# Kernel tuning notes

Measured on AMD Instinct MI355X. Metric: run time of the kernel, lower is better.

Reference implementation:

```python
import jax, jax.numpy as jnp
import numpy as np


def position_embedding(seq_len, d):
    # inv_freq_j = 1 / 10000^(2*j/d), pos_ij = sin(i * inv_freq_j)  -> [S, d]
    inv_freq = 1.0 / jnp.power(10000.0, 2.0 * jnp.arange(d, dtype=jnp.float32) / d)
    pos = jnp.arange(seq_len, dtype=jnp.float32)
    return jnp.sin(pos[:, None] * inv_freq[None, :])  # [S, d]


def setup_inputs() -> dict:
    key = jax.random.key(0)
    k1, k2 = jax.random.split(key)
    B, S, D, OUT = 4, 4096, 64, 64
    x = jax.random.normal(k1, (B, S, D), dtype=jnp.float32)
    kernel = jax.random.normal(k2, (3, D, OUT), dtype=jnp.float32) * 0.05
    return {"x": x, "kernel": kernel}


def reference(x, kernel):
    B, S, D = x.shape
    out_dim = kernel.shape[2]
    x = x + position_embedding(S, D)[None, :, :]  # broadcast pos-embed over batch
    # stacked QKV projection: [B,S,D] x [D,out] per slot
    wq = jnp.einsum('bsd,do->bso', x, kernel[0])
    wk = jnp.einsum('bsd,do->bso', x, kernel[1])
    wv = jnp.einsum('bsd,do->bso', x, kernel[2])
    scores = jnp.einsum('bso,bto->bst', wq, wk) / jnp.sqrt(jnp.asarray(out_dim, x.dtype))
    attn = jax.nn.softmax(scores, axis=-1)  # [B,S,S]
    return jnp.einsum('bst,bto->bso', attn, wv)
```

## Files before the change

kernel.cpp:

```cpp
#include <hip/hip_runtime.h>
#include <hip/hip_bf16.h>
#include <math.h>

using bf16x8 = __attribute__((ext_vector_type(8))) __bf16;
using bf16x4 = __attribute__((ext_vector_type(4))) __bf16;
using f32x4  = __attribute__((ext_vector_type(4))) float;
using f32x16 = __attribute__((ext_vector_type(16))) float;

static constexpr int SEQ = 4096;
static constexpr int DIM = 64;
static constexpr int NB  = 4;
static constexpr float QSCALE = 0.18033688011112042f;

__device__ __forceinline__ float fast_exp2(float x) {
#if __has_builtin(__builtin_amdgcn_exp2f)
    return __builtin_amdgcn_exp2f(x);
#else
    return exp2f(x);
#endif
}

__global__ __launch_bounds__(256)
void const_prep_kernel(const float* __restrict__ w, __bf16* __restrict__ WT,
                       float* __restrict__ peb)
{
    const int idx = (int)blockIdx.x * 256 + (int)threadIdx.x;
    const int spos = idx >> 6;
    const int c    = idx & 63;
    const float invf = exp2f(-13.287712379549449f * ((float)c * 0.03125f));
    peb[idx] = __sinf((float)spos * invf);
    if (idx < 3 * DIM * DIM) {
        const int s = idx >> 12;
        const int o = (idx >> 6) & 63;
        const int d = idx & 63;
        WT[idx] = (__bf16)w[(s * DIM + d) * DIM + o];
    }
}

__global__ __launch_bounds__(256)
void qkv_prep_kernel(const float* __restrict__ x, const __bf16* __restrict__ WT,
                     const float* __restrict__ peb,
                     __bf16* __restrict__ Qf, __bf16* __restrict__ Kf,
                     __bf16* __restrict__ Vf)
{
    const int tid  = (int)threadIdx.x;
    const int lane = tid & 63;
    const int g  = lane >> 4;
    const int cl = lane & 15;
    const int rowbase = (int)blockIdx.x * 64 + (tid >> 6) * 16;

    const int row  = rowbase + cl;
    const int spos = row & (SEQ - 1);
    bf16x8 xa[2];
#pragma unroll
    for (int h = 0; h < 2; ++h) {
        const float* xp = x + (long)row * DIM + 32*h + 8*g;
        const float* pp = peb + (long)spos * DIM + 32*h + 8*g;
        f32x4 x0 = *reinterpret_cast<const f32x4*>(xp);
        f32x4 x1 = *reinterpret_cast<const f32x4*>(xp + 4);
        f32x4 p0 = *reinterpret_cast<const f32x4*>(pp);
        f32x4 p1 = *reinterpret_cast<const f32x4*>(pp + 4);
        bf16x8 v;
#pragma unroll
        for (int e = 0; e < 8; ++e) {
            const float xv = (e < 4) ? x0[e] : x1[e - 4];
            const float pe = (e < 4) ? p0[e] : p1[e - 4];
            v[e] = (__bf16)(xv + pe);
        }
        xa[h] = v;
    }

    const int bi  = rowbase >> 12;
    const int sp  = rowbase & (SEQ - 1);
    const int c32 = sp >> 5;
    const int rb16 = sp & 16;

#pragma unroll
    for (int slot = 0; slot < 3; ++slot) {
        const __bf16* wt = WT + slot * DIM * DIM;
        f32x4 acc[4];
#pragma unroll
        for (int nt = 0; nt < 4; ++nt) acc[nt] = (f32x4){0.f, 0.f, 0.f, 0.f};
#pragma unroll
        for (int nt = 0; nt < 4; ++nt) {
            bf16x8 w0 = *reinterpret_cast<const bf16x8*>(wt + (nt*16 + cl) * DIM + 8*g);
            bf16x8 w1 = *reinterpret_cast<const bf16x8*>(wt + (nt*16 + cl) * DIM + 32 + 8*g);
            if (slot < 2) {
                acc[nt] = __builtin_amdgcn_mfma_f32_16x16x32_bf16(w0, xa[0], acc[nt], 0, 0, 0);
                acc[nt] = __builtin_amdgcn_mfma_f32_16x16x32_bf16(w1, xa[1], acc[nt], 0, 0, 0);
            } else {
                acc[nt] = __builtin_amdgcn_mfma_f32_16x16x32_bf16(xa[0], w0, acc[nt], 0, 0, 0);
                acc[nt] = __builtin_amdgcn_mfma_f32_16x16x32_bf16(xa[1], w1, acc[nt], 0, 0, 0);
            }
        }

        if (slot < 2) {
            __bf16* dst = (slot == 0) ? Qf : Kf;
            const float scale = (slot == 0) ? QSCALE : 1.0f;
            __bf16* base = dst + ((long)(bi*128 + c32) * 4) * 512
                         + (rb16 + cl + 32*(g >> 1)) * 8 + 4*(g & 1);
#pragma unroll
            for (int nt = 0; nt < 4; ++nt) {
                bf16x4 pk;
#pragma unroll
                for (int r = 0; r < 4; ++r) pk[r] = (__bf16)(acc[nt][r] * scale);
                *reinterpret_cast<bf16x4*>(base + nt*512) = pk;
            }
        } else {
            const int ks  = (sp >> 4) & 1;
            const int lde = (32*(g&1) + cl)*8 + (g>>1)*4;
            __bf16* vb = Vf + (((long)bi*128 + c32)*4 + ks*2)*512;
#pragma unroll
            for (int nt = 0; nt < 4; ++nt) {
                bf16x4 pk;
#pragma unroll
                for (int r = 0; r < 4; ++r) pk[r] = (__bf16)acc[nt][r];
                *reinterpret_cast<bf16x4*>(vb + (nt>>1)*512 + (nt&1)*128 + lde) = pk;
            }
        }
    }
}

__global__ __launch_bounds__(1024)
void attn_kernel(const __bf16* __restrict__ Qf, const __bf16* __restrict__ Kf,
                 const __bf16* __restrict__ Vf, float* __restrict__ out)
{
    __shared__ char smem[71680];
    float* lpart = (float*)smem;
    float* lms   = (float*)(smem + 69632);
    float* lls   = (float*)(smem + 70656);

    const int tid  = (int)threadIdx.x;
    const int w    = tid >> 6;
    const int lane = tid & 63;
    const int hi   = lane >> 5;
    const int l31  = lane & 31;
    const int qh   = w & 1;
    const int kq   = w >> 1;

    const int bid = (int)blockIdx.x;
    const int x8  = bid & 7;
    const int b   = x8 & 3;
    const int qt64 = ((x8 >> 2) << 5) | (bid >> 3);
    const int qt32 = qt64 * 2 + qh;

    const __bf16* Qfp = Qf + ((long)(b*128 + qt32)  * 4) * 512 + lane*8;
    const __bf16* Kfp = Kf + ((long)(b*128 + kq*16) * 4) * 512 + lane*8;
    const __bf16* Vfp = Vf + ((long)(b*128 + kq*16) * 4) * 512 + lane*8;

    bf16x8 qf[4];
#pragma unroll
    for (int d4 = 0; d4 < 4; ++d4)
        qf[d4] = *reinterpret_cast<const bf16x8*>(Qfp + d4*512);

    f32x16 acc[2];
#pragma unroll
    for (int dt = 0; dt < 2; ++dt)
#pragma unroll
        for (int r = 0; r < 16; ++r) acc[dt][r] = 0.f;
    float mrun = -INFINITY;
    float lsum = 0.f;

    bf16x8 kc0 = *reinterpret_cast<const bf16x8*>(Kfp);
    bf16x8 kc1 = *reinterpret_cast<const bf16x8*>(Kfp + 512);
    bf16x8 kc2 = *reinterpret_cast<const bf16x8*>(Kfp + 1024);
    bf16x8 kc3 = *reinterpret_cast<const bf16x8*>(Kfp + 1536);

#pragma unroll 2
    for (int n = 0; n < 16; ++n) {
        bf16x8 vc0 = *reinterpret_cast<const bf16x8*>(Vfp + n*2048);
        bf16x8 vc1 = *reinterpret_cast<const bf16x8*>(Vfp + n*2048 + 512);
        bf16x8 vc2 = *reinterpret_cast<const bf16x8*>(Vfp + n*2048 + 1024);
        bf16x8 vc3 = *reinterpret_cast<const bf16x8*>(Vfp + n*2048 + 1536);
        bf16x8 kn0, kn1, kn2, kn3;
        if (n < 15) {
            kn0 = *reinterpret_cast<const bf16x8*>(Kfp + (n+1)*2048);
            kn1 = *reinterpret_cast<const bf16x8*>(Kfp + (n+1)*2048 + 512);
        }

        f32x16 s;
#pragma unroll
        for (int r = 0; r < 16; ++r) s[r] = 0.f;
        __builtin_amdgcn_s_setprio(1);
        s = __builtin_amdgcn_mfma_f32_32x32x16_bf16(kc0, qf[0], s, 0, 0, 0);
        s = __builtin_amdgcn_mfma_f32_32x32x16_bf16(kc1, qf[1], s, 0, 0, 0);
        s = __builtin_amdgcn_mfma_f32_32x32x16_bf16(kc2, qf[2], s, 0, 0, 0);
        s = __builtin_amdgcn_mfma_f32_32x32x16_bf16(kc3, qf[3], s, 0, 0, 0);
        __builtin_amdgcn_s_setprio(0);

        if (n < 15) {
            kn2 = *reinterpret_cast<const bf16x8*>(Kfp + (n+1)*2048 + 1024);
            kn3 = *reinterpret_cast<const bf16x8*>(Kfp + (n+1)*2048 + 1536);
        }

        float t0 = fmaxf(fmaxf(s[0],  s[1]),  s[2]);
        float t1 = fmaxf(fmaxf(s[3],  s[4]),  s[5]);
        float t2 = fmaxf(fmaxf(s[6],  s[7]),  s[8]);
        float t3 = fmaxf(fmaxf(s[9],  s[10]), s[11]);
        float t4 = fmaxf(fmaxf(s[12], s[13]), s[14]);
        float tmax = fmaxf(fmaxf(fmaxf(t0, t1), t2), fmaxf(fmaxf(t3, t4), s[15]));
        tmax = fmaxf(tmax, __shfl_xor(tmax, 32));

        if (!__all(tmax <= mrun)) {
            const float mnew = fmaxf(mrun, tmax);
            const float corr = fast_exp2(mrun - mnew);
            lsum *= corr;
#pragma unroll
            for (int r = 0; r < 16; ++r) {
                acc[0][r] *= corr;
                acc[1][r] *= corr;
            }
            mrun = mnew;
        }

        float ps0 = 0.f, ps1 = 0.f, ps2 = 0.f, ps3 = 0.f;
#pragma unroll
        for (int r = 0; r < 4; ++r) {
            const float p0 = fast_exp2(s[r]      - mrun);
            const float p1 = fast_exp2(s[4 + r]  - mrun);
            const float p2 = fast_exp2(s[8 + r]  - mrun);
            const float p3 = fast_exp2(s[12 + r] - mrun);
            s[r] = p0; s[4 + r] = p1; s[8 + r] = p2; s[12 + r] = p3;
            ps0 += p0; ps1 += p1; ps2 += p2; ps3 += p3;
        }
        lsum += (ps0 + ps1) + (ps2 + ps3);

        bf16x8 pb0, pb1;
#pragma unroll
        for (int e = 0; e < 8; ++e) { pb0[e] = (__bf16)s[e]; pb1[e] = (__bf16)s[8 + e]; }

        __builtin_amdgcn_s_setprio(1);
        acc[0] = __builtin_amdgcn_mfma_f32_32x32x16_bf16(vc0, pb0, acc[0], 0, 0, 0);
        acc[1] = __builtin_amdgcn_mfma_f32_32x32x16_bf16(vc1, pb0, acc[1], 0, 0, 0);
        acc[0] = __builtin_amdgcn_mfma_f32_32x32x16_bf16(vc2, pb1, acc[0], 0, 0, 0);
        acc[1] = __builtin_amdgcn_mfma_f32_32x32x16_bf16(vc3, pb1, acc[1], 0, 0, 0);
        __builtin_amdgcn_s_setprio(0);

        kc0 = kn0; kc1 = kn1; kc2 = kn2; kc3 = kn3;
    }

    lsum += __shfl_xor(lsum, 32);

    auto write_slot = [&](int sl) {
        if (lane < 32) { lms[sl*32 + l31] = mrun; lls[sl*32 + l31] = lsum; }
        float* pp = lpart + sl*2176 + l31*68;
#pragma unroll
        for (int dt = 0; dt < 2; ++dt)
#pragma unroll
            for (int j = 0; j < 4; ++j) {
                f32x4 v;
#pragma unroll
                for (int c = 0; c < 4; ++c) v[c] = acc[dt][4*j + c];
                *reinterpret_cast<f32x4*>(pp + dt*32 + 8*j + 4*hi) = v;
            }
    };
    auto merge_slot = [&](int sl) {
        const float mp = lms[sl*32 + l31];
        const float lp = lls[sl*32 + l31];
        const float M  = fmaxf(mrun, mp);
        const float fo = fast_exp2(mrun - M);
        const float fp = fast_exp2(mp - M);
        lsum = lsum*fo + lp*fp;
        mrun = M;
        const float* pp = lpart + sl*2176 + l31*68;
#pragma unroll
        for (int dt = 0; dt < 2; ++dt)
#pragma unroll
            for (int j = 0; j < 4; ++j) {
                f32x4 v = *reinterpret_cast<const f32x4*>(pp + dt*32 + 8*j + 4*hi);
#pragma unroll
                for (int c = 0; c < 4; ++c)
                    acc[dt][4*j + c] = acc[dt][4*j + c]*fo + v[c]*fp;
            }
    };

    const int sb = qh * 4;
    if (kq >= 4) write_slot(sb + kq - 4);
    __syncthreads();
    if (kq < 4) merge_slot(sb + kq);
    if (kq == 2 || kq == 3) write_slot(sb + kq);
    __syncthreads();
    if (kq < 2) merge_slot(sb + kq + 2);
    if (kq == 1) write_slot(sb + 1);
    __syncthreads();
    if (kq == 0) {
        merge_slot(sb + 1);
        const float inv = 1.f / lsum;
#pragma unroll
        for (int dt = 0; dt < 2; ++dt)
#pragma unroll
            for (int r = 0; r < 16; ++r) acc[dt][r] *= inv;
        write_slot(sb);
    }
    __syncthreads();

    {
        const int q  = tid >> 4;
        const int dq = (tid & 15) * 4;
        const float* src = lpart + ((q >> 5) * 4) * 2176 + (q & 31) * 68 + dq;
        f32x4 o = *reinterpret_cast<const f32x4*>(src);
        *reinterpret_cast<f32x4*>(out + ((long)b * SEQ + qt64*64 + q) * DIM + dq) = o;
    }
}

extern "C" void kernel_launch(void* const* d_in, const int* in_sizes, int n_in,
                              void* d_out, int out_size, void* d_ws, size_t ws_size,
                              hipStream_t stream)
{
    const float* x = (const float*)d_in[0];
    const float* w = (const float*)d_in[1];
    float* out = (float*)d_out;

    char* ws = (char*)d_ws;
    const size_t sz = (size_t)NB * SEQ * DIM * sizeof(__bf16);
    __bf16* Qf  = (__bf16*)(ws);
    __bf16* Kf  = (__bf16*)(ws + sz);
    __bf16* Vf  = (__bf16*)(ws + 2 * sz);
    __bf16* WT  = (__bf16*)(ws + 3 * sz);
    float*  peb = (float*)(ws + 3 * sz + 32 * 1024);

    const_prep_kernel<<<SEQ * DIM / 256, 256, 0, stream>>>(w, WT, peb);

    qkv_prep_kernel<<<NB * SEQ / 64, 256, 0, stream>>>(x, WT, peb, Qf, Kf, Vf);

    attn_kernel<<<NB * SEQ / 64, 1024, 0, stream>>>(Qf, Kf, Vf, out);
}
```

Before: 48.31 us.

## Software-pipeline QK^T of next tile ahead of softmax/PV of current tile

Restructures the attention inner loop so the QK^T MFMAs for tile n+1 are computed right after the softmax and PV of tile n, using two ping-pong score buffers (sA/sB). The loop is manually unrolled by two with unroll 1. The aim is to overlap the MFMA work of the next score tile with the exp and reduction work of the current one, and to hide K load latency. The extra live f32x16 score buffer raises register pressure and could lower occupancy. The compiler may also just serialize the dependent sections anyway.

Result: slower. 65.15 us (+34.9%).

```diff
diff --git a/kernel.cpp b/kernel.cpp
--- a/kernel.cpp
+++ b/kernel.cpp
@@ -161,37 +161,22 @@
     float mrun = -INFINITY;
     float lsum = 0.f;
 
-    bf16x8 kc0 = *reinterpret_cast<const bf16x8*>(Kfp);
-    bf16x8 kc1 = *reinterpret_cast<const bf16x8*>(Kfp + 512);
-    bf16x8 kc2 = *reinterpret_cast<const bf16x8*>(Kfp + 1024);
-    bf16x8 kc3 = *reinterpret_cast<const bf16x8*>(Kfp + 1536);
-
-#pragma unroll 2
-    for (int n = 0; n < 16; ++n) {
+    auto qk_tile = [&](f32x16& s, bf16x8 k0, bf16x8 k1, bf16x8 k2, bf16x8 k3) {
+#pragma unroll
+        for (int r = 0; r < 16; ++r) s[r] = 0.f;
+        __builtin_amdgcn_s_setprio(1);
+        s = __builtin_amdgcn_mfma_f32_32x32x16_bf16(k0, qf[0], s, 0, 0, 0);
+        s = __builtin_amdgcn_mfma_f32_32x32x16_bf16(k1, qf[1], s, 0, 0, 0);
+        s = __builtin_amdgcn_mfma_f32_32x32x16_bf16(k2, qf[2], s, 0, 0, 0);
+        s = __builtin_amdgcn_mfma_f32_32x32x16_bf16(k3, qf[3], s, 0, 0, 0);
+        __builtin_amdgcn_s_setprio(0);
+    };
+
+    auto sm_pv = [&](f32x16& s, int n) {
         bf16x8 vc0 = *reinterpret_cast<const bf16x8*>(Vfp + n*2048);
         bf16x8 vc1 = *reinterpret_cast<const bf16x8*>(Vfp + n*2048 + 512);
         bf16x8 vc2 = *reinterpret_cast<const bf16x8*>(Vfp + n*2048 + 1024);
         bf16x8 vc3 = *reinterpret_cast<const bf16x8*>(Vfp + n*2048 + 1536);
-        bf16x8 kn0, kn1, kn2, kn3;
-        if (n < 15) {
-            kn0 = *reinterpret_cast<const bf16x8*>(Kfp + (n+1)*2048);
-            kn1 = *reinterpret_cast<const bf16x8*>(Kfp + (n+1)*2048 + 512);
-        }
-
-        f32x16 s;
-#pragma unroll
-        for (int r = 0; r < 16; ++r) s[r] = 0.f;
-        __builtin_amdgcn_s_setprio(1);
-        s = __builtin_amdgcn_mfma_f32_32x32x16_bf16(kc0, qf[0], s, 0, 0, 0);
-        s = __builtin_amdgcn_mfma_f32_32x32x16_bf16(kc1, qf[1], s, 0, 0, 0);
-        s = __builtin_amdgcn_mfma_f32_32x32x16_bf16(kc2, qf[2], s, 0, 0, 0);
-        s = __builtin_amdgcn_mfma_f32_32x32x16_bf16(kc3, qf[3], s, 0, 0, 0);
-        __builtin_amdgcn_s_setprio(0);
-
-        if (n < 15) {
-            kn2 = *reinterpret_cast<const bf16x8*>(Kfp + (n+1)*2048 + 1024);
-            kn3 = *reinterpret_cast<const bf16x8*>(Kfp + (n+1)*2048 + 1536);
-        }
 
         float t0 = fmaxf(fmaxf(s[0],  s[1]),  s[2]);
         float t1 = fmaxf(fmaxf(s[3],  s[4]),  s[5]);
@@ -235,8 +220,37 @@
         acc[0] = __builtin_amdgcn_mfma_f32_32x32x16_bf16(vc2, pb1, acc[0], 0, 0, 0);
         acc[1] = __builtin_amdgcn_mfma_f32_32x32x16_bf16(vc3, pb1, acc[1], 0, 0, 0);
         __builtin_amdgcn_s_setprio(0);
-
-        kc0 = kn0; kc1 = kn1; kc2 = kn2; kc3 = kn3;
+    };
+
+    f32x16 sA;
+    {
+        bf16x8 p0 = *reinterpret_cast<const bf16x8*>(Kfp);
+        bf16x8 p1 = *reinterpret_cast<const bf16x8*>(Kfp + 512);
+        bf16x8 p2 = *reinterpret_cast<const bf16x8*>(Kfp + 1024);
+        bf16x8 p3 = *reinterpret_cast<const bf16x8*>(Kfp + 1536);
+        qk_tile(sA, p0, p1, p2, p3);
+    }
+
+#pragma unroll 1
+    for (int n = 0; n < 16; n += 2) {
+        bf16x8 kB0 = *reinterpret_cast<const bf16x8*>(Kfp + (n+1)*2048);
+        bf16x8 kB1 = *reinterpret_cast<const bf16x8*>(Kfp + (n+1)*2048 + 512);
+        bf16x8 kB2 = *reinterpret_cast<const bf16x8*>(Kfp + (n+1)*2048 + 1024);
+        bf16x8 kB3 = *reinterpret_cast<const bf16x8*>(Kfp + (n+1)*2048 + 1536);
+        sm_pv(sA, n);
+        f32x16 sB;
+        qk_tile(sB, kB0, kB1, kB2, kB3);
+
+        if (n < 14) {
+            bf16x8 kA0 = *reinterpret_cast<const bf16x8*>(Kfp + (n+2)*2048);
+            bf16x8 kA1 = *reinterpret_cast<const bf16x8*>(Kfp + (n+2)*2048 + 512);
+            bf16x8 kA2 = *reinterpret_cast<const bf16x8*>(Kfp + (n+2)*2048 + 1024);
+            bf16x8 kA3 = *reinterpret_cast<const bf16x8*>(Kfp + (n+2)*2048 + 1536);
+            sm_pv(sB, n + 1);
+            qk_tile(sA, kA0, kA1, kA2, kA3);
+        } else {
+            sm_pv(sB, n + 1);
+        }
     }
 
     lsum += __shfl_xor(lsum, 32);
```
